# Optimization experiments

Hardware: AMD Instinct MI355X
Metric: run time of the kernel (lower is better)

## Reference

```python
import jax, jax.numpy as jnp
import numpy as np

SEQ, B, IN, H = 2048, 4096, 1, 32


def setup_inputs() -> dict:
    key = jax.random.key(0)
    ks = jax.random.split(key, 8)
    s_ih = 1.0 / np.sqrt(H)  # torch nn.RNN init scale
    return {
        "x": jax.random.normal(ks[0], (SEQ, B, IN), dtype=jnp.float32),
        "hidden": jnp.zeros((1, B, H), dtype=jnp.float32),
        "W_ih": jax.random.uniform(ks[1], (H, IN), jnp.float32, -s_ih, s_ih),
        "b_ih": jax.random.uniform(ks[2], (H,), jnp.float32, -s_ih, s_ih),
        "W_hh": jax.random.uniform(ks[3], (H, H), jnp.float32, -s_ih, s_ih),
        "b_hh": jax.random.uniform(ks[4], (H,), jnp.float32, -s_ih, s_ih),
        "W_fc": jax.random.uniform(ks[5], (IN, H), jnp.float32, -s_ih, s_ih),
        "b_fc": jax.random.uniform(ks[6], (IN,), jnp.float32, -s_ih, s_ih),
    }


def reference(x, hidden, W_ih, b_ih, W_hh, b_hh, W_fc, b_fc):
    # Elman RNN: h_t = tanh(x_t W_ih^T + b_ih + h_{t-1} W_hh^T + b_hh)
    # Precompute the input projection for all timesteps in one GEMM.
    x_proj = jnp.einsum('sbi,hi->sbh', x, W_ih) + b_ih + b_hh  # (SEQ, B, H)
    h0 = hidden[0]  # (B, H), single layer

    def step(h, xp_t):
        h_new = jnp.tanh(xp_t + h @ W_hh.T)
        return h_new, h_new

    _, outputs = jax.lax.scan(step, h0, x_proj)  # outputs: (SEQ, B, H)
    # Trailing Linear: (SEQ, B, H) -> (SEQ, B, IN)
    return jnp.einsum('sbh,oh->sbo', outputs, W_fc) + b_fc
```

## Files before the change

### kernel.cpp

```cpp
#include <hip/hip_runtime.h>

#define SEQ   2048
#define BATCH 4096
#define HD    32

typedef float f32x2 __attribute__((ext_vector_type(2)));
typedef float f32x4 __attribute__((ext_vector_type(4)));

__device__ __forceinline__ float exp2_fast(float a) {
#if __has_builtin(__builtin_amdgcn_exp2f)
    return __builtin_amdgcn_exp2f(a);
#else
    return exp2f(a);
#endif
}

__device__ __forceinline__ float rcp_fast(float a) {
#if __has_builtin(__builtin_amdgcn_rcpf)
    return __builtin_amdgcn_rcpf(a);
#else
    return 1.0f / a;
#endif
}

__device__ __forceinline__ float fast_tanh(float v) {
    float ax = fabsf(v);
    float e  = exp2_fast(ax * -2.8853900817779268f);
    float r  = (1.0f - e) * rcp_fast(1.0f + e);
    return copysignf(r, v);
}

template <int CTRL>
__device__ __forceinline__ float dpp_x(float v) {
    return __int_as_float(
        __builtin_amdgcn_update_dpp(0, __float_as_int(v), CTRL, 0xF, 0xF, false));
}

__device__ __forceinline__ float swz_xor16(float v) {
    return __int_as_float(__builtin_amdgcn_ds_swizzle(__float_as_int(v), 0x401F));
}

__global__
__attribute__((amdgpu_flat_work_group_size(512, 512)))
__attribute__((amdgpu_waves_per_eu(2, 2)))
void rnn_elman_kernel(
    const float* __restrict__ x, const float* __restrict__ hidden,
    const float* __restrict__ W_ih, const float* __restrict__ b_ih,
    const float* __restrict__ W_hh, const float* __restrict__ b_hh,
    const float* __restrict__ W_fc, const float* __restrict__ b_fc,
    float* __restrict__ out)
{
    __shared__ float sh[16 * 36];

    const int tid = threadIdx.x;
    const int i   = tid & 31;
    const int ks  = i & 3;
    const int eb  = tid >> 5;
    const int e   = blockIdx.x * 16 + eb;

    f32x2 wv[4][4];
    {
        const int rbase = i & ~3;
        #pragma unroll
        for (int j = 0; j < 4; ++j) {
            const float* R = W_hh + (rbase | (ks ^ j)) * HD + ks * 8;
            #pragma unroll
            for (int m = 0; m < 4; ++m) wv[j][m] = f32x2{R[2 * m], R[2 * m + 1]};
        }
    }
    const float wih  = W_ih[i];
    const float bias = b_ih[i] + b_hh[i];
    const float wfc  = W_fc[i];
    const float bfc  = b_fc[0];

    float* slot = sh + eb * 36;
    const f32x4* rd = reinterpret_cast<const f32x4*>(slot + ks * 8);

    slot[i] = hidden[e * HD + i];
    __builtin_amdgcn_wave_barrier();
    f32x2 h2[4];
    {
        const f32x4 a = rd[0], b = rd[1];
        h2[0] = f32x2{a.x, a.y}; h2[1] = f32x2{a.z, a.w};
        h2[2] = f32x2{b.x, b.y}; h2[3] = f32x2{b.z, b.w};
    }

    const float* __restrict__ xe = x + e;
    float xq0 = xe[(size_t)0 * BATCH];
    float xq1 = xe[(size_t)1 * BATCH];
    float xq2 = xe[(size_t)2 * BATCH];
    float xq3 = xe[(size_t)3 * BATCH];

    #pragma unroll 4
    for (int t = 0; t < SEQ; ++t) {
        const float xv = xq0;
        xq0 = xq1; xq1 = xq2; xq2 = xq3;
        {
            int tt = t + 4; tt = tt < SEQ ? tt : SEQ - 1;
            xq3 = xe[(size_t)tt * BATCH];
        }

        f32x2 p0 = f32x2{fmaf(xv, wih, bias), 0.f};
        f32x2 p1 = f32x2{0.f, 0.f};
        f32x2 p2 = f32x2{0.f, 0.f};
        f32x2 p3 = f32x2{0.f, 0.f};
        #pragma unroll
        for (int m = 0; m < 4; ++m) {
            const f32x2 hm = h2[m];
            p0 += wv[0][m] * hm;
            p1 += wv[1][m] * hm;
            p2 += wv[2][m] * hm;
            p3 += wv[3][m] * hm;
        }
        const float P0 = p0.x + p0.y;
        const float P1 = p1.x + p1.y;
        const float P2 = p2.x + p2.y;
        const float P3 = p3.x + p3.y;

        const float q0 = P0 + dpp_x<0xB1>(P1);
        const float q1 = P2 + dpp_x<0xB1>(P3);
        const float z  = q0 + dpp_x<0x4E>(q1);
        const float h  = fast_tanh(z);

        float u = h * wfc;
        u += dpp_x<0xB1>(u);
        u += dpp_x<0x4E>(u);
        u += dpp_x<0x141>(u);
        u += dpp_x<0x140>(u);
        const float usw = swz_xor16(u);

        slot[i] = h;
        __builtin_amdgcn_wave_barrier();
        const f32x4 a = rd[0], b = rd[1];
        h2[0] = f32x2{a.x, a.y}; h2[1] = f32x2{a.z, a.w};
        h2[2] = f32x2{b.x, b.y}; h2[3] = f32x2{b.z, b.w};

        if ((tid & 31) == 0) out[(size_t)t * BATCH + e] = u + usw + bfc;
    }
}

extern "C" void kernel_launch(void* const* d_in, const int* in_sizes, int n_in,
                              void* d_out, int out_size, void* d_ws, size_t ws_size,
                              hipStream_t stream) {
    const float* x    = (const float*)d_in[0];
    const float* hid  = (const float*)d_in[1];
    const float* W_ih = (const float*)d_in[2];
    const float* b_ih = (const float*)d_in[3];
    const float* W_hh = (const float*)d_in[4];
    const float* b_hh = (const float*)d_in[5];
    const float* W_fc = (const float*)d_in[6];
    const float* b_fc = (const float*)d_in[7];
    float* out = (float*)d_out;

    dim3 grid(BATCH / 16);
    dim3 block(512);
    rnn_elman_kernel<<<grid, block, 0, stream>>>(x, hid, W_ih, b_ih, W_hh, b_hh,
                                                 W_fc, b_fc, out);
}
```

Before: 576.5 us.

## Map one batch element per full wave with split-K permlane reduction

Reassigns work so each 64-lane wave handles one batch element, with each lane computing half of a W_hh row dot product and combining halves via permlane32 swap. This halves per-step FMA chain length per lane and doubles the number of waves, raising occupancy to hide recurrence latency. Block size drops to 256 and output reduction uses permlane16 swap. Total arithmetic is unchanged but duplicated across lanes for tanh and output projection.

```diff
diff --git a/kernel.cpp b/kernel.cpp
--- a/kernel.cpp
+++ b/kernel.cpp
@@ -6,6 +6,7 @@
 
 typedef float f32x2 __attribute__((ext_vector_type(2)));
 typedef float f32x4 __attribute__((ext_vector_type(4)));
+typedef unsigned int uint2v __attribute__((ext_vector_type(2)));
 
 __device__ __forceinline__ float exp2_fast(float a) {
 #if __has_builtin(__builtin_amdgcn_exp2f)
@@ -40,9 +41,32 @@
     return __int_as_float(__builtin_amdgcn_ds_swizzle(__float_as_int(v), 0x401F));
 }
 
+__device__ __forceinline__ float xsum16(float v) {
+#if __has_builtin(__builtin_amdgcn_permlane16_swap)
+    uint2v r = __builtin_amdgcn_permlane16_swap(__float_as_uint(v), __float_as_uint(v),
+                                                false, false);
+    return __uint_as_float(r.x) + __uint_as_float(r.y);
+#else
+    return v + swz_xor16(v);
+#endif
+}
+
+__device__ __forceinline__ float xsum32(float v) {
+#if __has_builtin(__builtin_amdgcn_permlane32_swap)
+    uint2v r = __builtin_amdgcn_permlane32_swap(__float_as_uint(v), __float_as_uint(v),
+                                                false, false);
+    return __uint_as_float(r.x) + __uint_as_float(r.y);
+#else
+    const int addr = (((int)(threadIdx.x & 63) ^ 32) << 2);
+    const float o  = __int_as_float(
+        __builtin_amdgcn_ds_bpermute(addr, __float_as_int(v)));
+    return v + o;
+#endif
+}
+
 __global__
-__attribute__((amdgpu_flat_work_group_size(512, 512)))
-__attribute__((amdgpu_waves_per_eu(2, 2)))
+__attribute__((amdgpu_flat_work_group_size(256, 256)))
+__attribute__((amdgpu_waves_per_eu(4)))
 void rnn_elman_kernel(
     const float* __restrict__ x, const float* __restrict__ hidden,
     const float* __restrict__ W_ih, const float* __restrict__ b_ih,
@@ -50,40 +74,34 @@
     const float* __restrict__ W_fc, const float* __restrict__ b_fc,
     float* __restrict__ out)
 {
-    __shared__ float sh[16 * 36];
+    __shared__ float sh[4 * 36];
 
-    const int tid = threadIdx.x;
-    const int i   = tid & 31;
-    const int ks  = i & 3;
-    const int eb  = tid >> 5;
-    const int e   = blockIdx.x * 16 + eb;
+    const int tid   = threadIdx.x;
+    const int lane  = tid & 63;
+    const int r     = lane & 31;
+    const int khalf = lane >> 5;
+    const int wid   = tid >> 6;
+    const int e     = __builtin_amdgcn_readfirstlane(blockIdx.x * 4 + wid);
 
-    f32x2 wv[4][4];
+    f32x2 wv[8];
     {
-        const int rbase = i & ~3;
+        const float* Wr = W_hh + r * HD + khalf * 16;
         #pragma unroll
-        for (int j = 0; j < 4; ++j) {
-            const float* R = W_hh + (rbase | (ks ^ j)) * HD + ks * 8;
-            #pragma unroll
-            for (int m = 0; m < 4; ++m) wv[j][m] = f32x2{R[2 * m], R[2 * m + 1]};
-        }
+        for (int m = 0; m < 8; ++m) wv[m] = f32x2{Wr[2 * m], Wr[2 * m + 1]};
     }
-    const float wih  = W_ih[i];
-    const float bias = b_ih[i] + b_hh[i];
-    const float wfc  = W_fc[i];
-    const float bfc  = b_fc[0];
+    const float seedw = khalf ? 0.f : W_ih[r];
+    const float seedb = khalf ? 0.f : (b_ih[r] + b_hh[r]);
+    const float wfc   = W_fc[r];
+    const float bfc   = b_fc[0];
 
-    float* slot = sh + eb * 36;
-    const f32x4* rd = reinterpret_cast<const f32x4*>(slot + ks * 8);
+    float* slot = sh + wid * 36;
+    const f32x4* rd = reinterpret_cast<const f32x4*>(slot + khalf * 16);
 
-    slot[i] = hidden[e * HD + i];
+    slot[r] = hidden[e * HD + r];
     __builtin_amdgcn_wave_barrier();
-    f32x2 h2[4];
-    {
-        const f32x4 a = rd[0], b = rd[1];
-        h2[0] = f32x2{a.x, a.y}; h2[1] = f32x2{a.z, a.w};
-        h2[2] = f32x2{b.x, b.y}; h2[3] = f32x2{b.z, b.w};
-    }
+    f32x4 hb[4];
+    #pragma unroll
+    for (int m = 0; m < 4; ++m) hb[m] = rd[m];
 
     const float* __restrict__ xe = x + e;
     float xq0 = xe[(size_t)0 * BATCH];
@@ -100,42 +118,35 @@
             xq3 = xe[(size_t)tt * BATCH];
         }
 
-        f32x2 p0 = f32x2{fmaf(xv, wih, bias), 0.f};
-        f32x2 p1 = f32x2{0.f, 0.f};
-        f32x2 p2 = f32x2{0.f, 0.f};
-        f32x2 p3 = f32x2{0.f, 0.f};
+        const f32x2* h2 = reinterpret_cast<const f32x2*>(hb);
+        f32x2 p0 = wv[0] * h2[0];
+        f32x2 p1 = wv[1] * h2[1];
+        p0 += wv[2] * h2[2];
+        p1 += wv[3] * h2[3];
+        p0 += wv[4] * h2[4];
+        p1 += wv[5] * h2[5];
+        p0 += wv[6] * h2[6];
+        p1 += wv[7] * h2[7];
+        const f32x2 ps   = p0 + p1;
+        const float seed = fmaf(xv, seedw, seedb);
+        const float pmine = (ps.x + ps.y) + seed;
+
+        const float z = xsum32(pmine);
+        const float h = fast_tanh(z);
+
+        slot[r] = h;
+        __builtin_amdgcn_wave_barrier();
         #pragma unroll
-        for (int m = 0; m < 4; ++m) {
-            const f32x2 hm = h2[m];
-            p0 += wv[0][m] * hm;
-            p1 += wv[1][m] * hm;
-            p2 += wv[2][m] * hm;
-            p3 += wv[3][m] * hm;
-        }
-        const float P0 = p0.x + p0.y;
-        const float P1 = p1.x + p1.y;
-        const float P2 = p2.x + p2.y;
-        const float P3 = p3.x + p3.y;
-
-        const float q0 = P0 + dpp_x<0xB1>(P1);
-        const float q1 = P2 + dpp_x<0xB1>(P3);
-        const float z  = q0 + dpp_x<0x4E>(q1);
-        const float h  = fast_tanh(z);
+        for (int m = 0; m < 4; ++m) hb[m] = rd[m];
 
         float u = h * wfc;
         u += dpp_x<0xB1>(u);
         u += dpp_x<0x4E>(u);
         u += dpp_x<0x141>(u);
         u += dpp_x<0x140>(u);
-        const float usw = swz_xor16(u);
+        const float tot = xsum16(u) + bfc;
 
-        slot[i] = h;
-        __builtin_amdgcn_wave_barrier();
-        const f32x4 a = rd[0], b = rd[1];
-        h2[0] = f32x2{a.x, a.y}; h2[1] = f32x2{a.z, a.w};
-        h2[2] = f32x2{b.x, b.y}; h2[3] = f32x2{b.z, b.w};
-
-        if ((tid & 31) == 0) out[(size_t)t * BATCH + e] = u + usw + bfc;
+        if (lane == 0) out[(size_t)t * BATCH + e] = tot;
     }
 }
 
@@ -152,8 +163,8 @@
     const float* b_fc = (const float*)d_in[7];
     float* out = (float*)d_out;
 
-    dim3 grid(BATCH / 16);
-    dim3 block(512);
+    dim3 grid(BATCH / 4);
+    dim3 block(256);
     rnn_elman_kernel<<<grid, block, 0, stream>>>(x, hid, W_ih, b_ih, W_hh, b_hh,
                                                  W_fc, b_fc, out);
 }
```

Measured after the change: 792.4 us. +37.5%, slower.

## Fuse DPP reductions, use permlane16 swap, defer output reduction past LDS exchange

Applied to the files above, without the earlier changes.

The output-projection reduction now runs after the hidden state is written to LDS and reloaded, taking it off the serial recurrence path. The reduction uses inline-asm v_add_f32_dpp with quad_perm and mirror patterns, so each step is a single instruction instead of a separate DPP move plus add. The final cross-16 step uses permlane16_swap when available instead of ds_swizzle, avoiding an LDS-path round trip. Weights become named registers and the matvec uses explicit packed FMAs. The inline asm may limit how freely the compiler schedules these instructions.

```diff
diff --git a/kernel.cpp b/kernel.cpp
--- a/kernel.cpp
+++ b/kernel.cpp
@@ -6,6 +6,7 @@
 
 typedef float f32x2 __attribute__((ext_vector_type(2)));
 typedef float f32x4 __attribute__((ext_vector_type(4)));
+typedef unsigned int uint2v __attribute__((ext_vector_type(2)));
 
 __device__ __forceinline__ float exp2_fast(float a) {
 #if __has_builtin(__builtin_amdgcn_exp2f)
@@ -36,8 +37,37 @@
         __builtin_amdgcn_update_dpp(0, __float_as_int(v), CTRL, 0xF, 0xF, false));
 }
 
+#define ADD_DPP_QP(u, A, B, Cc, D)                                          \
+    asm("v_add_f32_dpp %0, %1, %2 quad_perm:[" #A "," #B "," #Cc "," #D     \
+        "] row_mask:0xf bank_mask:0xf"                                      \
+        : "=v"(u) : "v"(u), "v"(u))
+#define ADD_DPP_HM(u)                                                       \
+    asm("v_add_f32_dpp %0, %1, %2 row_half_mirror row_mask:0xf bank_mask:0xf" \
+        : "=v"(u) : "v"(u), "v"(u))
+#define ADD_DPP_M(u)                                                        \
+    asm("v_add_f32_dpp %0, %1, %2 row_mirror row_mask:0xf bank_mask:0xf"    \
+        : "=v"(u) : "v"(u), "v"(u))
+
 __device__ __forceinline__ float swz_xor16(float v) {
     return __int_as_float(__builtin_amdgcn_ds_swizzle(__float_as_int(v), 0x401F));
+}
+
+__device__ __forceinline__ float xsum16(float v) {
+#if __has_builtin(__builtin_amdgcn_permlane16_swap)
+    uint2v r = __builtin_amdgcn_permlane16_swap(__float_as_uint(v), __float_as_uint(v),
+                                                false, false);
+    return __uint_as_float(r.x) + __uint_as_float(r.y);
+#else
+    return v + swz_xor16(v);
+#endif
+}
+
+__device__ __forceinline__ f32x2 pk_fma(f32x2 a, f32x2 b, f32x2 c) {
+#if __has_builtin(__builtin_elementwise_fma)
+    return __builtin_elementwise_fma(a, b, c);
+#else
+    return f32x2{fmaf(a.x, b.x, c.x), fmaf(a.y, b.y, c.y)};
+#endif
 }
 
 __global__
@@ -58,32 +88,27 @@
     const int eb  = tid >> 5;
     const int e   = blockIdx.x * 16 + eb;
 
-    f32x2 wv[4][4];
-    {
-        const int rbase = i & ~3;
-        #pragma unroll
-        for (int j = 0; j < 4; ++j) {
-            const float* R = W_hh + (rbase | (ks ^ j)) * HD + ks * 8;
-            #pragma unroll
-            for (int m = 0; m < 4; ++m) wv[j][m] = f32x2{R[2 * m], R[2 * m + 1]};
-        }
-    }
-    const float wih  = W_ih[i];
-    const float bias = b_ih[i] + b_hh[i];
-    const float wfc  = W_fc[i];
-    const float bfc  = b_fc[0];
+    const int rbase = i & ~3;
+    const f32x2* R0 = reinterpret_cast<const f32x2*>(W_hh + (rbase | (ks ^ 0)) * HD + ks * 8);
+    const f32x2* R1 = reinterpret_cast<const f32x2*>(W_hh + (rbase | (ks ^ 1)) * HD + ks * 8);
+    const f32x2* R2 = reinterpret_cast<const f32x2*>(W_hh + (rbase | (ks ^ 2)) * HD + ks * 8);
+    const f32x2* R3 = reinterpret_cast<const f32x2*>(W_hh + (rbase | (ks ^ 3)) * HD + ks * 8);
+    const f32x2 w0a = R0[0], w0b = R0[1], w0c = R0[2], w0d = R0[3];
+    const f32x2 w1a = R1[0], w1b = R1[1], w1c = R1[2], w1d = R1[3];
+    const f32x2 w2a = R2[0], w2b = R2[1], w2c = R2[2], w2d = R2[3];
+    const f32x2 w3a = R3[0], w3b = R3[1], w3c = R3[2], w3d = R3[3];
+
+    const float seedw = W_ih[i];
+    const float bias  = b_ih[i] + b_hh[i];
+    const float wfc   = W_fc[i];
+    const float bfc   = b_fc[0];
 
     float* slot = sh + eb * 36;
     const f32x4* rd = reinterpret_cast<const f32x4*>(slot + ks * 8);
 
     slot[i] = hidden[e * HD + i];
     __builtin_amdgcn_wave_barrier();
-    f32x2 h2[4];
-    {
-        const f32x4 a = rd[0], b = rd[1];
-        h2[0] = f32x2{a.x, a.y}; h2[1] = f32x2{a.z, a.w};
-        h2[2] = f32x2{b.x, b.y}; h2[3] = f32x2{b.z, b.w};
-    }
+    f32x4 A = rd[0], B = rd[1];
 
     const float* __restrict__ xe = x + e;
     float xq0 = xe[(size_t)0 * BATCH];
@@ -97,21 +122,27 @@
         xq0 = xq1; xq1 = xq2; xq2 = xq3;
         {
             int tt = t + 4; tt = tt < SEQ ? tt : SEQ - 1;
-            xq3 = xe[(size_t)tt * BATCH];
+            const float* xr = x + (size_t)tt * BATCH;
+            xq3 = xr[e];
         }
+        const float seed = fmaf(xv, seedw, bias);
 
-        f32x2 p0 = f32x2{fmaf(xv, wih, bias), 0.f};
+        const f32x2 h0 = __builtin_shufflevector(A, A, 0, 1);
+        const f32x2 h1 = __builtin_shufflevector(A, A, 2, 3);
+        const f32x2 h2 = __builtin_shufflevector(B, B, 0, 1);
+        const f32x2 h3 = __builtin_shufflevector(B, B, 2, 3);
+        f32x2 p0 = f32x2{seed, 0.f};
         f32x2 p1 = f32x2{0.f, 0.f};
         f32x2 p2 = f32x2{0.f, 0.f};
         f32x2 p3 = f32x2{0.f, 0.f};
-        #pragma unroll
-        for (int m = 0; m < 4; ++m) {
-            const f32x2 hm = h2[m];
-            p0 += wv[0][m] * hm;
-            p1 += wv[1][m] * hm;
-            p2 += wv[2][m] * hm;
-            p3 += wv[3][m] * hm;
-        }
+        p0 = pk_fma(w0a, h0, p0); p1 = pk_fma(w1a, h0, p1);
+        p2 = pk_fma(w2a, h0, p2); p3 = pk_fma(w3a, h0, p3);
+        p0 = pk_fma(w0b, h1, p0); p1 = pk_fma(w1b, h1, p1);
+        p2 = pk_fma(w2b, h1, p2); p3 = pk_fma(w3b, h1, p3);
+        p0 = pk_fma(w0c, h2, p0); p1 = pk_fma(w1c, h2, p1);
+        p2 = pk_fma(w2c, h2, p2); p3 = pk_fma(w3c, h2, p3);
+        p0 = pk_fma(w0d, h3, p0); p1 = pk_fma(w1d, h3, p1);
+        p2 = pk_fma(w2d, h3, p2); p3 = pk_fma(w3d, h3, p3);
         const float P0 = p0.x + p0.y;
         const float P1 = p1.x + p1.y;
         const float P2 = p2.x + p2.y;
@@ -122,20 +153,18 @@
         const float z  = q0 + dpp_x<0x4E>(q1);
         const float h  = fast_tanh(z);
 
-        float u = h * wfc;
-        u += dpp_x<0xB1>(u);
-        u += dpp_x<0x4E>(u);
-        u += dpp_x<0x141>(u);
-        u += dpp_x<0x140>(u);
-        const float usw = swz_xor16(u);
-
         slot[i] = h;
         __builtin_amdgcn_wave_barrier();
-        const f32x4 a = rd[0], b = rd[1];
-        h2[0] = f32x2{a.x, a.y}; h2[1] = f32x2{a.z, a.w};
-        h2[2] = f32x2{b.x, b.y}; h2[3] = f32x2{b.z, b.w};
+        A = rd[0]; B = rd[1];
 
-        if ((tid & 31) == 0) out[(size_t)t * BATCH + e] = u + usw + bfc;
+        float u = h * wfc;
+        ADD_DPP_QP(u, 1, 0, 3, 2);
+        ADD_DPP_QP(u, 2, 3, 0, 1);
+        ADD_DPP_HM(u);
+        ADD_DPP_M(u);
+        const float tot = xsum16(u) + bfc;
+
+        if ((tid & 31) == 0) out[(size_t)t * BATCH + e] = tot;
     }
 }
 
```

Measured after the change: 573.2 us. Within noise of the previous version (-0.6%).
